# Kernel tuning notes

Hardware: AMD Instinct MI355X
Metric: run time of the kernel (lower is better)

Reference implementation:

```python
import jax, jax.numpy as jnp
import numpy as np

HEADS = 8
DIM_HEAD = 64
SCALE = DIM_HEAD ** -0.5


def setup_inputs() -> dict:
    key = jax.random.key(0)
    k1, k2, k3, k4 = jax.random.split(key, 4)
    b, n, dim = 2, 2048, 512
    inner = HEADS * DIM_HEAD  # 512
    x = jax.random.normal(k1, (b, n, dim), dtype=jnp.float32)
    adj = jax.random.uniform(k2, (b, n, n), dtype=jnp.float32)
    w_qkv = jax.random.normal(k3, (dim, 3 * inner), dtype=jnp.float32) * (dim ** -0.5)
    w_out = jax.random.normal(k4, (inner, dim), dtype=jnp.float32) * (inner ** -0.5)
    b_out = jnp.zeros((dim,), dtype=jnp.float32)
    return {"x": x, "adj": adj, "w_qkv": w_qkv, "w_out": w_out, "b_out": b_out}


def reference(x, adj, w_qkv, w_out, b_out):
    b, n, dim = x.shape
    qkv = x @ w_qkv  # [b, n, 3*inner]
    q, k, v = jnp.split(qkv, 3, axis=-1)
    # [b, n, h*d] -> [b, h, n, d]
    reshape = lambda t: t.reshape(b, n, HEADS, DIM_HEAD).transpose(0, 2, 1, 3)
    q, k, v = reshape(q), reshape(k), reshape(v)
    dots = jnp.einsum('bhid,bhjd->bhij', q, k) * SCALE  # [b, h, n, n]
    # softmax over adjacency rows, broadcast across heads, multiply into scores
    mask = jax.nn.softmax(adj, axis=-1)[:, None, :, :]  # [b, 1, n, n]
    attn = jax.nn.softmax(mask * dots, axis=-1)
    out = jnp.einsum('bhij,bhjd->bhid', attn, v)  # [b, h, n, d]
    out = out.transpose(0, 2, 1, 3).reshape(b, n, HEADS * DIM_HEAD)
    return out @ w_out + b_out
```

## Files before the change

### kernel.cpp

```cpp
#include <hip/hip_runtime.h>
#include <hip/hip_bf16.h>
#include <math.h>

#define BB 2
#define NN 2048
#define DIM 512
#define NH 8
#define HD 64
#define SCALE 0.125f

typedef __bf16 bf16x8 __attribute__((ext_vector_type(8)));
typedef __bf16 bf16x4 __attribute__((ext_vector_type(4)));
typedef float floatx4 __attribute__((ext_vector_type(4)));

static inline __device__ floatx4 mfma16(bf16x8 a, bf16x8 b, floatx4 c) {
    return __builtin_amdgcn_mfma_f32_16x16x32_bf16(a, b, c, 0, 0, 0);
}

static inline __device__ bf16x8 cvt8(float4 a, float4 b) {
    bf16x8 r;
    r[0] = (__bf16)a.x; r[1] = (__bf16)a.y; r[2] = (__bf16)a.z; r[3] = (__bf16)a.w;
    r[4] = (__bf16)b.x; r[5] = (__bf16)b.y; r[6] = (__bf16)b.z; r[7] = (__bf16)b.w;
    return r;
}

static inline __device__ float bf2f(unsigned short u) {
    return __uint_as_float(((unsigned)u) << 16);
}

static inline __device__ void dma16(const void* g, void* l) {
    __builtin_amdgcn_global_load_lds(
        (const __attribute__((address_space(1))) unsigned int*)g,
        (__attribute__((address_space(3))) unsigned int*)l,
        16, 0, 0);
}

__global__ __launch_bounds__(256) void adj_softmax(const float* __restrict__ adj,
                                                   __bf16* __restrict__ mask) {
    int row = blockIdx.x;
    const float* a = adj + (size_t)row * NN;
    __bf16* m = mask + (size_t)row * NN;
    int t = threadIdx.x;
    float4 va = *(const float4*)(a + 4 * t);
    float4 vb = *(const float4*)(a + 1024 + 4 * t);
    float v[8] = {va.x, va.y, va.z, va.w, vb.x, vb.y, vb.z, vb.w};
    float mx = -INFINITY;
#pragma unroll
    for (int c = 0; c < 8; ++c) mx = fmaxf(mx, v[c]);
    __shared__ float red[256];
    red[t] = mx; __syncthreads();
    for (int s = 128; s > 0; s >>= 1) {
        if (t < s) red[t] = fmaxf(red[t], red[t + s]);
        __syncthreads();
    }
    mx = red[0]; __syncthreads();
    float sm = 0.f;
    float e[8];
#pragma unroll
    for (int c = 0; c < 8; ++c) { e[c] = __expf(v[c] - mx); sm += e[c]; }
    red[t] = sm; __syncthreads();
    for (int s = 128; s > 0; s >>= 1) {
        if (t < s) red[t] += red[t + s];
        __syncthreads();
    }
    float inv = 1.0f / red[0];
    bf16x4 o0, o1;
#pragma unroll
    for (int c = 0; c < 4; ++c) { o0[c] = (__bf16)(e[c] * inv); o1[c] = (__bf16)(e[c + 4] * inv); }
    *(bf16x4*)(m + 4 * t) = o0;
    *(bf16x4*)(m + 1024 + 4 * t) = o1;
}

__global__ __launch_bounds__(256) void xcast(const float* __restrict__ x,
                                             __bf16* __restrict__ xb) {
    int g = blockIdx.x * 256 + threadIdx.x;
    float4 f0 = ((const float4*)x)[2 * (size_t)g];
    float4 f1 = ((const float4*)x)[2 * (size_t)g + 1];
    *(bf16x8*)(xb + 8 * (size_t)g) = cvt8(f0, f1);
}

__global__ __launch_bounds__(256) void tcast_w(const float* __restrict__ w,
                                               __bf16* __restrict__ wT,
                                               int K, int N) {
    __shared__ float tile[32][33];
    int n0 = blockIdx.x * 32, k0 = blockIdx.y * 32;
    int c = threadIdx.x & 31, r = threadIdx.x >> 5;
#pragma unroll
    for (int p = 0; p < 4; ++p)
        tile[r + p * 8][c] = w[(size_t)(k0 + r + p * 8) * N + n0 + c];
    __syncthreads();
#pragma unroll
    for (int p = 0; p < 4; ++p)
        wT[(size_t)(n0 + r + p * 8) * K + k0 + c] = (__bf16)tile[c][r + p * 8];
}

__global__ __launch_bounds__(256) void qkv_mfma(const __bf16* __restrict__ xb,
                                                const __bf16* __restrict__ wT,
                                                __bf16* __restrict__ q,
                                                __bf16* __restrict__ kk,
                                                __bf16* __restrict__ vT) {
    __shared__ __bf16 As[128 * 32];
    __shared__ __bf16 Bs[64 * 32];
    const int t = threadIdx.x;
    const int lane = t & 63, w = t >> 6;
    const int n16 = lane & 15, quad = lane >> 4;
    const int wm = w >> 1, wn = w & 1;
    const int m0 = blockIdx.y * 128, n0 = blockIdx.x * 64;

    const int drow = t >> 2;
    const int dchunk = (t & 3) ^ (drow & 3);
    char* ldsA = (char*)As + (t >> 6) * 1024;
    char* ldsB = (char*)Bs + (t >> 6) * 1024;

    floatx4 acc[4][2];
#pragma unroll
    for (int mt = 0; mt < 4; ++mt)
#pragma unroll
        for (int nt = 0; nt < 2; ++nt) acc[mt][nt] = (floatx4){0.f, 0.f, 0.f, 0.f};

    const int swz = n16 & 3;

    for (int k0 = 0; k0 < 512; k0 += 32) {
        __syncthreads();
        dma16(xb + (size_t)(m0 + drow) * 512 + k0 + dchunk * 8, ldsA);
        dma16(xb + (size_t)(m0 + 64 + drow) * 512 + k0 + dchunk * 8, (char*)As + 4096 + (t >> 6) * 1024);
        dma16(wT + (size_t)(n0 + drow) * 512 + k0 + dchunk * 8, ldsB);
        __syncthreads();
        bf16x8 af[4], bf[2];
#pragma unroll
        for (int mt = 0; mt < 4; ++mt)
            af[mt] = *(const bf16x8*)(As + (wm * 64 + mt * 16 + n16) * 32 + (quad ^ swz) * 8);
#pragma unroll
        for (int nt = 0; nt < 2; ++nt)
            bf[nt] = *(const bf16x8*)(Bs + (wn * 32 + nt * 16 + n16) * 32 + (quad ^ swz) * 8);
#pragma unroll
        for (int mt = 0; mt < 4; ++mt)
#pragma unroll
            for (int nt = 0; nt < 2; ++nt)
                acc[mt][nt] = mfma16(af[mt], bf[nt], acc[mt][nt]);
    }

#pragma unroll
    for (int mt = 0; mt < 4; ++mt)
#pragma unroll
        for (int nt = 0; nt < 2; ++nt)
#pragma unroll
            for (int r = 0; r < 4; ++r) {
                int m = m0 + wm * 64 + mt * 16 + quad * 4 + r;
                int n = n0 + wn * 32 + nt * 16 + n16;
                int b = m >> 11, i = m & 2047;
                int sg = n >> 9, cc = n & 511;
                int h = cc >> 6, d = cc & 63;
                size_t bh = (size_t)(b * NH + h);
                float fv = acc[mt][nt][r];
                if (sg == 0)      q[(bh * NN + i) * HD + d] = (__bf16)(fv * SCALE);
                else if (sg == 1) kk[(bh * NN + i) * HD + d] = (__bf16)fv;
                else              vT[(bh * HD + d) * NN + i] = (__bf16)fv;
            }
}

__global__ __launch_bounds__(256, 4) void flash_attn(const __bf16* __restrict__ qb,
                                                     const __bf16* __restrict__ kb,
                                                     const __bf16* __restrict__ vTb,
                                                     const __bf16* __restrict__ maskb,
                                                     __bf16* __restrict__ Opart,
                                                     float* __restrict__ lpart) {
    __shared__ __bf16 Ks[64][72];
    __shared__ __bf16 Vs[64][72];
    __shared__ __bf16 Ps[64][72];

    const int t = threadIdx.x;
    const int lane = t & 63;
    const int w = t >> 6;
    const int n16 = lane & 15;
    const int quad = lane >> 4;

    const int blk = blockIdx.x;
    const int split = blk & 3;
    const int it = (blk >> 2) & 31;
    const int h = (blk >> 7) & 7;
    const int b = blk >> 10;
    const int i0 = it * 64;
    const int bh = b * NH + h;

    bf16x8 qfrag[2];
    {
        const __bf16* qrow = qb + ((size_t)bh * NN + i0 + w * 16 + n16) * HD;
        qfrag[0] = *(const bf16x8*)(qrow + quad * 8);
        qfrag[1] = *(const bf16x8*)(qrow + 32 + quad * 8);
    }

    floatx4 O[4];
#pragma unroll
    for (int dt = 0; dt < 4; ++dt) O[dt] = (floatx4){0.f, 0.f, 0.f, 0.f};
    float lp = 0.f;

    const int srow = t >> 3, sseg = t & 7;
    const __bf16* kg = kb + (size_t)bh * NN * HD;
    const __bf16* vg = vTb + (size_t)bh * HD * NN;
    const __bf16* mbase = maskb + ((size_t)b * NN + i0 + w * 16 + n16) * NN;

    int j0 = split * (NN / 4);
    float4 k1 = *(const float4*)(kg + (size_t)(j0 + srow) * HD + sseg * 8);
    float4 k2 = *(const float4*)(kg + (size_t)(j0 + srow + 32) * HD + sseg * 8);
    float4 v1 = *(const float4*)(vg + (size_t)srow * NN + j0 + sseg * 8);
    float4 v2 = *(const float4*)(vg + (size_t)(srow + 32) * NN + j0 + sseg * 8);

    for (int iter = 0; iter < (NN / 4) / 64; ++iter, j0 += 64) {
        __syncthreads();
        *(float4*)(&Ks[srow][sseg * 8]) = k1;
        *(float4*)(&Ks[srow + 32][sseg * 8]) = k2;
        *(float4*)(&Vs[srow][sseg * 8]) = v1;
        *(float4*)(&Vs[srow + 32][sseg * 8]) = v2;
        __syncthreads();
        if (iter + 1 < (NN / 4) / 64) {
            int jn = j0 + 64;
            k1 = *(const float4*)(kg + (size_t)(jn + srow) * HD + sseg * 8);
            k2 = *(const float4*)(kg + (size_t)(jn + srow + 32) * HD + sseg * 8);
            v1 = *(const float4*)(vg + (size_t)srow * NN + jn + sseg * 8);
            v2 = *(const float4*)(vg + (size_t)(srow + 32) * NN + jn + sseg * 8);
        }
        ushort4 mu[4];
        const __bf16* mrow = mbase + j0 + quad * 4;
#pragma unroll
        for (int jt = 0; jt < 4; ++jt)
            mu[jt] = *(const ushort4*)(mrow + jt * 16);

        floatx4 S[4];
#pragma unroll
        for (int jt = 0; jt < 4; ++jt) {
            floatx4 acc = (floatx4){0.f, 0.f, 0.f, 0.f};
            bf16x8 kf0 = *(const bf16x8*)(&Ks[jt * 16 + n16][quad * 8]);
            bf16x8 kf1 = *(const bf16x8*)(&Ks[jt * 16 + n16][32 + quad * 8]);
            acc = mfma16(kf0, qfrag[0], acc);
            acc = mfma16(kf1, qfrag[1], acc);
            S[jt] = acc;
        }

#pragma unroll
        for (int jt = 0; jt < 4; ++jt) {
            float p0 = __expf(S[jt][0] * bf2f(mu[jt].x));
            float p1 = __expf(S[jt][1] * bf2f(mu[jt].y));
            float p2 = __expf(S[jt][2] * bf2f(mu[jt].z));
            float p3 = __expf(S[jt][3] * bf2f(mu[jt].w));
            lp += (p0 + p1) + (p2 + p3);
            bf16x4 pk;
            pk[0] = (__bf16)p0; pk[1] = (__bf16)p1;
            pk[2] = (__bf16)p2; pk[3] = (__bf16)p3;
            *(bf16x4*)(&Ps[w * 16 + n16][jt * 16 + quad * 4]) = pk;
        }

        bf16x8 pf0 = *(const bf16x8*)(&Ps[w * 16 + n16][quad * 8]);
        bf16x8 pf1 = *(const bf16x8*)(&Ps[w * 16 + n16][32 + quad * 8]);
#pragma unroll
        for (int dt = 0; dt < 4; ++dt) {
            bf16x8 vf0 = *(const bf16x8*)(&Vs[dt * 16 + n16][quad * 8]);
            bf16x8 vf1 = *(const bf16x8*)(&Vs[dt * 16 + n16][32 + quad * 8]);
            O[dt] = mfma16(pf0, vf0, O[dt]);
            O[dt] = mfma16(pf1, vf1, O[dt]);
        }
    }

    lp += __shfl_xor(lp, 16);
    lp += __shfl_xor(lp, 32);
    const size_t sb = (size_t)(split * BB * NH + bh);
    if (quad == 0)
        lpart[sb * NN + i0 + w * 16 + n16] = lp;
#pragma unroll
    for (int dt = 0; dt < 4; ++dt)
#pragma unroll
        for (int r = 0; r < 4; ++r) {
            int i = i0 + w * 16 + quad * 4 + r;
            int d = dt * 16 + n16;
            Opart[(sb * NN + i) * HD + d] = (__bf16)O[dt][r];
        }
}

__global__ __launch_bounds__(256) void combine(const __bf16* __restrict__ Opart,
                                               const float* __restrict__ lpart,
                                               __bf16* __restrict__ ohb) {
    int g = blockIdx.x * 256 + threadIdx.x;
    int d0 = (g & 7) * 8;
    int n = (g >> 3) & 2047;
    int bh = g >> 14;
    int b = bh >> 3, h = bh & 7;
    float o[8] = {};
    float l = 0.f;
#pragma unroll
    for (int s = 0; s < 4; ++s) {
        size_t sb = (size_t)(s * BB * NH + bh);
        bf16x8 ov = *(const bf16x8*)(Opart + (sb * NN + n) * HD + d0);
#pragma unroll
        for (int e = 0; e < 8; ++e) o[e] += (float)ov[e];
        l += lpart[sb * NN + n];
    }
    float inv = 1.0f / l;
    bf16x8 r;
#pragma unroll
    for (int e = 0; e < 8; ++e) r[e] = (__bf16)(o[e] * inv);
    *(bf16x8*)(ohb + ((size_t)b * NN + n) * (NH * HD) + h * HD + d0) = r;
}

__global__ __launch_bounds__(256) void out_mfma(const __bf16* __restrict__ A,
                                                const __bf16* __restrict__ wT,
                                                const float* __restrict__ bias,
                                                float* __restrict__ out) {
    __shared__ __bf16 As[64 * 32];
    __shared__ __bf16 Bs[128 * 32];
    const int t = threadIdx.x;
    const int lane = t & 63, w = t >> 6;
    const int n16 = lane & 15, quad = lane >> 4;
    const int wm = w >> 1, wn = w & 1;
    const int m0 = blockIdx.y * 64, n0 = blockIdx.x * 128;

    const int drow = t >> 2;
    const int dchunk = (t & 3) ^ (drow & 3);
    char* ldsA = (char*)As + (t >> 6) * 1024;
    char* ldsB = (char*)Bs + (t >> 6) * 1024;
    const int swz = n16 & 3;

    floatx4 acc[2][4];
#pragma unroll
    for (int mt = 0; mt < 2; ++mt)
#pragma unroll
        for (int nt = 0; nt < 4; ++nt) acc[mt][nt] = (floatx4){0.f, 0.f, 0.f, 0.f};

    for (int k0 = 0; k0 < 512; k0 += 32) {
        __syncthreads();
        dma16(A + (size_t)(m0 + drow) * 512 + k0 + dchunk * 8, ldsA);
        dma16(wT + (size_t)(n0 + drow) * 512 + k0 + dchunk * 8, ldsB);
        dma16(wT + (size_t)(n0 + 64 + drow) * 512 + k0 + dchunk * 8, (char*)Bs + 4096 + (t >> 6) * 1024);
        __syncthreads();
        bf16x8 af[2], bf[4];
#pragma unroll
        for (int mt = 0; mt < 2; ++mt)
            af[mt] = *(const bf16x8*)(As + (wm * 32 + mt * 16 + n16) * 32 + (quad ^ swz) * 8);
#pragma unroll
        for (int nt = 0; nt < 4; ++nt)
            bf[nt] = *(const bf16x8*)(Bs + (wn * 64 + nt * 16 + n16) * 32 + (quad ^ swz) * 8);
#pragma unroll
        for (int mt = 0; mt < 2; ++mt)
#pragma unroll
            for (int nt = 0; nt < 4; ++nt)
                acc[mt][nt] = mfma16(af[mt], bf[nt], acc[mt][nt]);
    }

#pragma unroll
    for (int mt = 0; mt < 2; ++mt)
#pragma unroll
        for (int nt = 0; nt < 4; ++nt)
#pragma unroll
            for (int r = 0; r < 4; ++r) {
                int m = m0 + wm * 32 + mt * 16 + quad * 4 + r;
                int n = n0 + wn * 64 + nt * 16 + n16;
                out[(size_t)m * 512 + n] = acc[mt][nt][r] + bias[n];
            }
}

extern "C" void kernel_launch(void* const* d_in, const int* in_sizes, int n_in,
                              void* d_out, int out_size, void* d_ws, size_t ws_size,
                              hipStream_t stream) {
    const float* x     = (const float*)d_in[0];
    const float* adj   = (const float*)d_in[1];
    const float* w_qkv = (const float*)d_in[2];
    const float* w_out = (const float*)d_in[3];
    const float* b_out = (const float*)d_in[4];
    float* out = (float*)d_out;
    char* wsb = (char*)d_ws;

    __bf16* wqkvT = (__bf16*)(wsb + 0);
    __bf16* woutT = (__bf16*)(wsb + (3u << 19));
    __bf16* q     = (__bf16*)(wsb + (2u << 20));
    __bf16* ohb   = (__bf16*)(wsb + (2u << 20));
    __bf16* k     = (__bf16*)(wsb + (6u << 20));
    __bf16* vT    = (__bf16*)(wsb + (10u << 20));
    __bf16* mask  = (__bf16*)(wsb + (14u << 20));
    __bf16* Opart = (__bf16*)(wsb + (30u << 20));
    __bf16* xb    = (__bf16*)(wsb + (30u << 20));
    float*  lpart = (float*) (wsb + (46u << 20));

    adj_softmax<<<BB * NN, 256, 0, stream>>>(adj, mask);
    xcast<<<1024, 256, 0, stream>>>(x, xb);
    tcast_w<<<dim3(1536 / 32, 512 / 32), 256, 0, stream>>>(w_qkv, wqkvT, 512, 1536);
    tcast_w<<<dim3(512 / 32, 512 / 32), 256, 0, stream>>>(w_out, woutT, 512, 512);
    qkv_mfma<<<dim3(1536 / 64, 4096 / 128), 256, 0, stream>>>(xb, wqkvT, q, k, vT);
    flash_attn<<<BB * NH * 32 * 4, 256, 0, stream>>>(q, k, vT, mask, Opart, lpart);
    combine<<<1024, 256, 0, stream>>>(Opart, lpart, ohb);
    out_mfma<<<dim3(512 / 128, 4096 / 64), 256, 0, stream>>>(ohb, woutT, b_out, out);
}
```

Before: 175.7 us.

## Use wave shuffles in adj softmax, deepen GEMM K tiles, halve attention split

```diff
diff --git a/kernel.cpp b/kernel.cpp
--- a/kernel.cpp
+++ b/kernel.cpp
@@ -41,29 +41,28 @@
     const float* a = adj + (size_t)row * NN;
     __bf16* m = mask + (size_t)row * NN;
     int t = threadIdx.x;
+    int w = t >> 6, lane = t & 63;
     float4 va = *(const float4*)(a + 4 * t);
     float4 vb = *(const float4*)(a + 1024 + 4 * t);
     float v[8] = {va.x, va.y, va.z, va.w, vb.x, vb.y, vb.z, vb.w};
     float mx = -INFINITY;
 #pragma unroll
     for (int c = 0; c < 8; ++c) mx = fmaxf(mx, v[c]);
-    __shared__ float red[256];
-    red[t] = mx; __syncthreads();
-    for (int s = 128; s > 0; s >>= 1) {
-        if (t < s) red[t] = fmaxf(red[t], red[t + s]);
-        __syncthreads();
-    }
-    mx = red[0]; __syncthreads();
+#pragma unroll
+    for (int s = 1; s < 64; s <<= 1) mx = fmaxf(mx, __shfl_xor(mx, s));
+    __shared__ float red[8];
+    if (lane == 0) red[w] = mx;
+    __syncthreads();
+    mx = fmaxf(fmaxf(red[0], red[1]), fmaxf(red[2], red[3]));
     float sm = 0.f;
     float e[8];
 #pragma unroll
     for (int c = 0; c < 8; ++c) { e[c] = __expf(v[c] - mx); sm += e[c]; }
-    red[t] = sm; __syncthreads();
-    for (int s = 128; s > 0; s >>= 1) {
-        if (t < s) red[t] += red[t + s];
-        __syncthreads();
-    }
-    float inv = 1.0f / red[0];
+#pragma unroll
+    for (int s = 1; s < 64; s <<= 1) sm += __shfl_xor(sm, s);
+    if (lane == 0) red[4 + w] = sm;
+    __syncthreads();
+    float inv = 1.0f / ((red[4] + red[5]) + (red[6] + red[7]));
     bf16x4 o0, o1;
 #pragma unroll
     for (int c = 0; c < 4; ++c) { o0[c] = (__bf16)(e[c] * inv); o1[c] = (__bf16)(e[c + 4] * inv); }
@@ -99,18 +98,18 @@
                                                 __bf16* __restrict__ q,
                                                 __bf16* __restrict__ kk,
                                                 __bf16* __restrict__ vT) {
-    __shared__ __bf16 As[128 * 32];
-    __shared__ __bf16 Bs[64 * 32];
+    __shared__ __bf16 As[128 * 64];
+    __shared__ __bf16 Bs[64 * 64];
     const int t = threadIdx.x;
     const int lane = t & 63, w = t >> 6;
     const int n16 = lane & 15, quad = lane >> 4;
     const int wm = w >> 1, wn = w & 1;
     const int m0 = blockIdx.y * 128, n0 = blockIdx.x * 64;
 
-    const int drow = t >> 2;
-    const int dchunk = (t & 3) ^ (drow & 3);
-    char* ldsA = (char*)As + (t >> 6) * 1024;
-    char* ldsB = (char*)Bs + (t >> 6) * 1024;
+    const int srow = t >> 3;
+    const int schunk = (t & 7) ^ ((t >> 3) & 7);
+    const int woff = w * 1024;
+    const int rchunk = (n16 & 7);
 
     floatx4 acc[4][2];
 #pragma unroll
@@ -118,26 +117,33 @@
 #pragma unroll
         for (int nt = 0; nt < 2; ++nt) acc[mt][nt] = (floatx4){0.f, 0.f, 0.f, 0.f};
 
-    const int swz = n16 & 3;
-
-    for (int k0 = 0; k0 < 512; k0 += 32) {
-        __syncthreads();
-        dma16(xb + (size_t)(m0 + drow) * 512 + k0 + dchunk * 8, ldsA);
-        dma16(xb + (size_t)(m0 + 64 + drow) * 512 + k0 + dchunk * 8, (char*)As + 4096 + (t >> 6) * 1024);
-        dma16(wT + (size_t)(n0 + drow) * 512 + k0 + dchunk * 8, ldsB);
-        __syncthreads();
-        bf16x8 af[4], bf[2];
-#pragma unroll
-        for (int mt = 0; mt < 4; ++mt)
-            af[mt] = *(const bf16x8*)(As + (wm * 64 + mt * 16 + n16) * 32 + (quad ^ swz) * 8);
-#pragma unroll
-        for (int nt = 0; nt < 2; ++nt)
-            bf[nt] = *(const bf16x8*)(Bs + (wn * 32 + nt * 16 + n16) * 32 + (quad ^ swz) * 8);
-#pragma unroll
-        for (int mt = 0; mt < 4; ++mt)
+    for (int k0 = 0; k0 < 512; k0 += 64) {
+        __syncthreads();
+#pragma unroll
+        for (int d = 0; d < 4; ++d)
+            dma16(xb + (size_t)(m0 + d * 32 + srow) * 512 + k0 + schunk * 8,
+                  (char*)As + d * 4096 + woff);
+#pragma unroll
+        for (int d = 0; d < 2; ++d)
+            dma16(wT + (size_t)(n0 + d * 32 + srow) * 512 + k0 + schunk * 8,
+                  (char*)Bs + d * 4096 + woff);
+        __syncthreads();
+#pragma unroll
+        for (int kh = 0; kh < 2; ++kh) {
+            const int ch = (kh * 4 + quad) ^ rchunk;
+            bf16x8 af[4], bf[2];
+#pragma unroll
+            for (int mt = 0; mt < 4; ++mt)
+                af[mt] = *(const bf16x8*)(As + (wm * 64 + mt * 16 + n16) * 64 + ch * 8);
 #pragma unroll
             for (int nt = 0; nt < 2; ++nt)
-                acc[mt][nt] = mfma16(af[mt], bf[nt], acc[mt][nt]);
+                bf[nt] = *(const bf16x8*)(Bs + (wn * 32 + nt * 16 + n16) * 64 + ch * 8);
+#pragma unroll
+            for (int mt = 0; mt < 4; ++mt)
+#pragma unroll
+                for (int nt = 0; nt < 2; ++nt)
+                    acc[mt][nt] = mfma16(af[mt], bf[nt], acc[mt][nt]);
+        }
     }
 
 #pragma unroll
@@ -176,10 +182,10 @@
     const int quad = lane >> 4;
 
     const int blk = blockIdx.x;
-    const int split = blk & 3;
-    const int it = (blk >> 2) & 31;
-    const int h = (blk >> 7) & 7;
-    const int b = blk >> 10;
+    const int split = blk & 1;
+    const int it = (blk >> 1) & 31;
+    const int h = (blk >> 6) & 7;
+    const int b = blk >> 9;
     const int i0 = it * 64;
     const int bh = b * NH + h;
 
@@ -200,20 +206,20 @@
     const __bf16* vg = vTb + (size_t)bh * HD * NN;
     const __bf16* mbase = maskb + ((size_t)b * NN + i0 + w * 16 + n16) * NN;
 
-    int j0 = split * (NN / 4);
+    int j0 = split * (NN / 2);
     float4 k1 = *(const float4*)(kg + (size_t)(j0 + srow) * HD + sseg * 8);
     float4 k2 = *(const float4*)(kg + (size_t)(j0 + srow + 32) * HD + sseg * 8);
     float4 v1 = *(const float4*)(vg + (size_t)srow * NN + j0 + sseg * 8);
     float4 v2 = *(const float4*)(vg + (size_t)(srow + 32) * NN + j0 + sseg * 8);
 
-    for (int iter = 0; iter < (NN / 4) / 64; ++iter, j0 += 64) {
+    for (int iter = 0; iter < (NN / 2) / 64; ++iter, j0 += 64) {
         __syncthreads();
         *(float4*)(&Ks[srow][sseg * 8]) = k1;
         *(float4*)(&Ks[srow + 32][sseg * 8]) = k2;
         *(float4*)(&Vs[srow][sseg * 8]) = v1;
         *(float4*)(&Vs[srow + 32][sseg * 8]) = v2;
         __syncthreads();
-        if (iter + 1 < (NN / 4) / 64) {
+        if (iter + 1 < (NN / 2) / 64) {
             int jn = j0 + 64;
             k1 = *(const float4*)(kg + (size_t)(jn + srow) * HD + sseg * 8);
             k2 = *(const float4*)(kg + (size_t)(jn + srow + 32) * HD + sseg * 8);
@@ -284,20 +290,16 @@
     int n = (g >> 3) & 2047;
     int bh = g >> 14;
     int b = bh >> 3, h = bh & 7;
-    float o[8] = {};
-    float l = 0.f;
-#pragma unroll
-    for (int s = 0; s < 4; ++s) {
-        size_t sb = (size_t)(s * BB * NH + bh);
-        bf16x8 ov = *(const bf16x8*)(Opart + (sb * NN + n) * HD + d0);
-#pragma unroll
-        for (int e = 0; e < 8; ++e) o[e] += (float)ov[e];
-        l += lpart[sb * NN + n];
-    }
+    size_t idx0 = ((size_t)bh * NN + n) * HD + d0;
+    size_t idx1 = ((size_t)(BB * NH + bh) * NN + n) * HD + d0;
+    bf16x8 o0 = *(const bf16x8*)(Opart + idx0);
+    bf16x8 o1 = *(const bf16x8*)(Opart + idx1);
+    float l = lpart[(size_t)bh * NN + n] + lpart[(size_t)(BB * NH + bh) * NN + n];
     float inv = 1.0f / l;
     bf16x8 r;
 #pragma unroll
-    for (int e = 0; e < 8; ++e) r[e] = (__bf16)(o[e] * inv);
+    for (int e = 0; e < 8; ++e)
+        r[e] = (__bf16)(((float)o0[e] + (float)o1[e]) * inv);
     *(bf16x8*)(ohb + ((size_t)b * NN + n) * (NH * HD) + h * HD + d0) = r;
 }
 
@@ -305,54 +307,62 @@
                                                 const __bf16* __restrict__ wT,
                                                 const float* __restrict__ bias,
                                                 float* __restrict__ out) {
-    __shared__ __bf16 As[64 * 32];
-    __shared__ __bf16 Bs[128 * 32];
+    __shared__ __bf16 As[64 * 64];
+    __shared__ __bf16 Bs[64 * 64];
     const int t = threadIdx.x;
     const int lane = t & 63, w = t >> 6;
     const int n16 = lane & 15, quad = lane >> 4;
     const int wm = w >> 1, wn = w & 1;
-    const int m0 = blockIdx.y * 64, n0 = blockIdx.x * 128;
-
-    const int drow = t >> 2;
-    const int dchunk = (t & 3) ^ (drow & 3);
-    char* ldsA = (char*)As + (t >> 6) * 1024;
-    char* ldsB = (char*)Bs + (t >> 6) * 1024;
-    const int swz = n16 & 3;
-
-    floatx4 acc[2][4];
+    const int m0 = blockIdx.y * 64, n0 = blockIdx.x * 64;
+
+    const int srow = t >> 3;
+    const int schunk = (t & 7) ^ ((t >> 3) & 7);
+    const int woff = w * 1024;
+    const int rchunk = (n16 & 7);
+
+    floatx4 acc[2][2];
 #pragma unroll
     for (int mt = 0; mt < 2; ++mt)
 #pragma unroll
-        for (int nt = 0; nt < 4; ++nt) acc[mt][nt] = (floatx4){0.f, 0.f, 0.f, 0.f};
-
-    for (int k0 = 0; k0 < 512; k0 += 32) {
-        __syncthreads();
-        dma16(A + (size_t)(m0 + drow) * 512 + k0 + dchunk * 8, ldsA);
-        dma16(wT + (size_t)(n0 + drow) * 512 + k0 + dchunk * 8, ldsB);
-        dma16(wT + (size_t)(n0 + 64 + drow) * 512 + k0 + dchunk * 8, (char*)Bs + 4096 + (t >> 6) * 1024);
-        __syncthreads();
-        bf16x8 af[2], bf[4];
-#pragma unroll
-        for (int mt = 0; mt < 2; ++mt)
-            af[mt] = *(const bf16x8*)(As + (wm * 32 + mt * 16 + n16) * 32 + (quad ^ swz) * 8);
-#pragma unroll
-        for (int nt = 0; nt < 4; ++nt)
-            bf[nt] = *(const bf16x8*)(Bs + (wn * 64 + nt * 16 + n16) * 32 + (quad ^ swz) * 8);
-#pragma unroll
-        for (int mt = 0; mt < 2; ++mt)
-#pragma unroll
-            for (int nt = 0; nt < 4; ++nt)
-                acc[mt][nt] = mfma16(af[mt], bf[nt], acc[mt][nt]);
+        for (int nt = 0; nt < 2; ++nt) acc[mt][nt] = (floatx4){0.f, 0.f, 0.f, 0.f};
+
+    for (int k0 = 0; k0 < 512; k0 += 64) {
+        __syncthreads();
+#pragma unroll
+        for (int d = 0; d < 2; ++d)
+            dma16(A + (size_t)(m0 + d * 32 + srow) * 512 + k0 + schunk * 8,
+                  (char*)As + d * 4096 + woff);
+#pragma unroll
+        for (int d = 0; d < 2; ++d)
+            dma16(wT + (size_t)(n0 + d * 32 + srow) * 512 + k0 + schunk * 8,
+                  (char*)Bs + d * 4096 + woff);
+        __syncthreads();
+#pragma unroll
+        for (int kh = 0; kh < 2; ++kh) {
+            const int ch = (kh * 4 + quad) ^ rchunk;
+            bf16x8 af[2], bf[2];
+#pragma unroll
+            for (int mt = 0; mt < 2; ++mt)
+                af[mt] = *(const bf16x8*)(As + (wm * 32 + mt * 16 + n16) * 64 + ch * 8);
+#pragma unroll
+            for (int nt = 0; nt < 2; ++nt)
+                bf[nt] = *(const bf16x8*)(Bs + (wn * 32 + nt * 16 + n16) * 64 + ch * 8);
+#pragma unroll
+            for (int mt = 0; mt < 2; ++mt)
+#pragma unroll
+                for (int nt = 0; nt < 2; ++nt)
+                    acc[mt][nt] = mfma16(af[mt], bf[nt], acc[mt][nt]);
+        }
     }
 
 #pragma unroll
     for (int mt = 0; mt < 2; ++mt)
 #pragma unroll
-        for (int nt = 0; nt < 4; ++nt)
+        for (int nt = 0; nt < 2; ++nt)
 #pragma unroll
             for (int r = 0; r < 4; ++r) {
                 int m = m0 + wm * 32 + mt * 16 + quad * 4 + r;
-                int n = n0 + wn * 64 + nt * 16 + n16;
+                int n = n0 + wn * 32 + nt * 16 + n16;
                 out[(size_t)m * 512 + n] = acc[mt][nt][r] + bias[n];
             }
 }
@@ -384,7 +394,7 @@
     tcast_w<<<dim3(1536 / 32, 512 / 32), 256, 0, stream>>>(w_qkv, wqkvT, 512, 1536);
     tcast_w<<<dim3(512 / 32, 512 / 32), 256, 0, stream>>>(w_out, woutT, 512, 512);
     qkv_mfma<<<dim3(1536 / 64, 4096 / 128), 256, 0, stream>>>(xb, wqkvT, q, k, vT);
-    flash_attn<<<BB * NH * 32 * 4, 256, 0, stream>>>(q, k, vT, mask, Opart, lpart);
+    flash_attn<<<BB * NH * 32 * 2, 256, 0, stream>>>(q, k, vT, mask, Opart, lpart);
     combine<<<1024, 256, 0, stream>>>(Opart, lpart, ohb);
-    out_mfma<<<dim3(512 / 128, 4096 / 64), 256, 0, stream>>>(ohb, woutT, b_out, out);
-}
+    out_mfma<<<dim3(512 / 64, 4096 / 64), 256, 0, stream>>>(ohb, woutT, b_out, out);
+}
```

Measured after the change: 165.6 us. -5.7%, faster.
